# Kernel optimization log

Measured on AMD Instinct MI355X. Metric: run time of the kernel, lower is better.

The kernel has to match this reference:

```python
import math
import jax, jax.numpy as jnp
import numpy as np

B, S, D, H = 2, 2048, 1024, 16
HD = D // H  # 64


def setup_inputs() -> dict:
    key = jax.random.key(0)
    k = jax.random.split(key, 8)
    x = jax.random.normal(k[0], (B, S, D), dtype=jnp.float32)
    # RoPE tables: inv_freq over half dim, emb = concat(freqs, freqs)
    inv_freq = 1.0 / (10000.0 ** (jnp.arange(0, HD, 2, dtype=jnp.float32) / HD))
    pos = jnp.arange(S, dtype=jnp.float32)
    freqs = pos[:, None] * inv_freq[None, :]            # [S, HD/2]
    emb = jnp.concatenate([freqs, freqs], axis=-1)      # [S, HD]
    cos = jnp.cos(emb)[:, None, :]                      # [S, 1, HD] broadcasts over [B,S,H,HD]
    sin = jnp.sin(emb)[:, None, :]
    # causal additive mask [1, 1, S, S]
    neg = jnp.finfo(jnp.float32).min
    mask = jnp.where(jnp.tril(jnp.ones((S, S), dtype=bool)), 0.0, neg)[None, None]
    scale = 0.02
    wq = jax.random.normal(k[1], (D, D), dtype=jnp.float32) * scale
    wk = jax.random.normal(k[2], (D, D), dtype=jnp.float32) * scale
    wv = jax.random.normal(k[3], (D, D), dtype=jnp.float32) * scale
    wo = jax.random.normal(k[4], (D, D), dtype=jnp.float32) * scale
    return {"x": x, "cos": cos, "sin": sin, "mask": mask,
            "wq": wq, "wk": wk, "wv": wv, "wo": wo}


def rotate_half(t):
    t1, t2 = t[..., : t.shape[-1] // 2], t[..., t.shape[-1] // 2:]
    return jnp.concatenate([-t2, t1], axis=-1)


def reference(x, cos, sin, mask, wq, wk, wv, wo):
    b, s, d = x.shape
    # torch nn.Linear: y = x @ W^T  (W is [out, in])
    q = (x @ wq.T).reshape(b, s, H, HD)
    kk = (x @ wk.T).reshape(b, s, H, HD)
    v = (x @ wv.T).reshape(b, s, H, HD)
    q = q * cos + rotate_half(q) * sin
    kk = kk * cos + rotate_half(kk) * sin
    q = q.transpose(0, 2, 1, 3)   # [b, h, s, hd]
    kk = kk.transpose(0, 2, 1, 3)
    v = v.transpose(0, 2, 1, 3)
    scores = jnp.einsum('bhqd,bhkd->bhqk', q, kk) / math.sqrt(HD)
    scores = scores + mask
    probs = jax.nn.softmax(scores.astype(jnp.float32), axis=-1).astype(q.dtype)
    out = jnp.einsum('bhqk,bhkd->bhqd', probs, v)
    out = out.transpose(0, 2, 1, 3).reshape(b, s, d)
    return out @ wo.T
```

## Files before the change

### kernel.cpp

```cpp
#include <hip/hip_runtime.h>
#include <hip/hip_bf16.h>

typedef __hip_bfloat16 bf16;
typedef unsigned short u16;
typedef __attribute__((ext_vector_type(8))) short short8;
typedef __attribute__((ext_vector_type(4))) float floatx4;

constexpr int B_ = 2, S_ = 2048, D_ = 1024, H_ = 16, HD_ = 64;
constexpr int QT = 64, KT = 64, PAD = 72;
constexpr int NQT = S_ / QT;
constexpr int GK = 1024, BK = 64;

__device__ inline float b2f(u16 u) {
    union { unsigned int i; float f; } v; v.i = ((unsigned int)u) << 16; return v.f;
}
__device__ inline u16 f2b(float f) {
    bf16 h = __float2bfloat16(f); return *(u16*)&h;
}

__device__ inline void gl16(const u16* g, u16* l) {
    __builtin_amdgcn_global_load_lds(
        (const __attribute__((address_space(1))) unsigned int*)g,
        (__attribute__((address_space(3))) unsigned int*)l, 16, 0, 0);
}

__global__ __launch_bounds__(256) void cvt_kernel(
    const float* __restrict__ x,  const float* __restrict__ wq,
    const float* __restrict__ wk, const float* __restrict__ wv,
    const float* __restrict__ wo,
    u16* __restrict__ Xb, u16* __restrict__ Wb)
{
    const size_t c = (size_t)blockIdx.x * 256 + threadIdx.x;
    const float* src; u16* dst; size_t off;
    if (c < (size_t)(1 << 19)) { src = x; dst = Xb; off = c; }
    else {
        const size_t w = c - (1 << 19);
        const int wi = (int)(w >> 17);
        off = w & ((1 << 17) - 1);
        src = (wi == 0) ? wq : (wi == 1) ? wk : (wi == 2) ? wv : wo;
        dst = Wb + ((size_t)wi << 20);
    }
    const float4 a = *(const float4*)(src + off * 8);
    const float4 b = *(const float4*)(src + off * 8 + 4);
    ushort4 u0; u0.x = f2b(a.x); u0.y = f2b(a.y); u0.z = f2b(a.z); u0.w = f2b(a.w);
    ushort4 u1; u1.x = f2b(b.x); u1.y = f2b(b.y); u1.z = f2b(b.z); u1.w = f2b(b.w);
    *(ushort4*)(dst + off * 8)     = u0;
    *(ushort4*)(dst + off * 8 + 4) = u1;
}

template <typename TC, int SCATTER, int ROPE, int BN>
__global__ __launch_bounds__(256) void gemm_async(
    const u16* __restrict__ A, const u16* __restrict__ Wb,
    const float* __restrict__ cosp, const float* __restrict__ sinp,
    TC* __restrict__ C0, TC* __restrict__ C1, TC* __restrict__ C2, int N)
{
    constexpr int NT = BN / 32;

    int x, y, z;
    {
        const int xcd = blockIdx.x & 7, idx = blockIdx.x >> 3;
        y = (xcd & 3) * 8 + (idx & 7);
        if (BN == 128) {
            const int xz = (xcd >> 2) * 12 + (idx >> 3);
            x = xz & 7; z = xz >> 3;
        } else {
            x = (xcd >> 2) * 8 + (idx >> 3);
            z = 0;
        }
    }

    const u16* W = Wb + ((size_t)z << 20);
    TC*        C = (z == 0) ? C0 : (z == 1 ? C1 : C2);

    __shared__ __align__(16) u16 As[128 * BK];
    __shared__ __align__(16) u16 Bs[BN * BK];

    const int tid  = threadIdx.x;
    const int wave = tid >> 6, lane = tid & 63;
    const int quad = lane >> 4, l16 = lane & 15;
    const int wm = wave >> 1, wn = wave & 1;
    const int m0 = y * 128, n0 = x * BN;

    const int srl = lane >> 3;
    const int sc  = (lane & 7) ^ srl;

    floatx4 acc[4][NT] = {};

    for (int k0 = 0; k0 < GK; k0 += BK) {
        __syncthreads();
#pragma unroll
        for (int j = 0; j < 4; ++j) {
            const int rb = wave * 32 + j * 8;
            gl16(A + (size_t)(m0 + rb + srl) * GK + k0 + sc * 8, &As[rb * BK]);
        }
#pragma unroll
        for (int j = 0; j < BN / 32; ++j) {
            const int rb = wave * (BN / 4) + j * 8;
            gl16(W + (size_t)(n0 + rb + srl) * GK + k0 + sc * 8, &Bs[rb * BK]);
        }
        __syncthreads();

#pragma unroll
        for (int ks = 0; ks < 2; ++ks) {
            short8 af[4], bfr[NT];
#pragma unroll
            for (int mt = 0; mt < 4; ++mt) {
                const int R = wm * 64 + mt * 16 + l16;
                af[mt] = *(const short8*)&As[R * BK + (((ks * 4 + quad) ^ (l16 & 7)) * 8)];
            }
#pragma unroll
            for (int nt = 0; nt < NT; ++nt) {
                const int R = wn * (BN / 2) + nt * 16 + l16;
                bfr[nt] = *(const short8*)&Bs[R * BK + (((ks * 4 + quad) ^ (l16 & 7)) * 8)];
            }
#pragma unroll
            for (int mt = 0; mt < 4; ++mt)
#pragma unroll
                for (int nt = 0; nt < NT; ++nt)
                    acc[mt][nt] = __builtin_amdgcn_mfma_f32_16x16x32_bf16(
                        af[mt], bfr[nt], acc[mt][nt], 0, 0, 0);
        }
    }

    if (ROPE && z < 2) {
        float* Cs = (float*)As;
        float* Sn = (float*)Bs;
        const int s0 = m0 & (S_ - 1);
        const int bq = m0 >> 11;
        __syncthreads();
        {
            const int rr = tid >> 1;
            const int cc = (tid & 1) * 16;
            const float4* cp = (const float4*)(cosp + (size_t)(s0 + rr) * HD_ + cc);
            const float4* sp = (const float4*)(sinp + (size_t)(s0 + rr) * HD_ + cc);
            float4* cd = (float4*)&Cs[rr * 32 + cc];
            float4* sd = (float4*)&Sn[rr * 32 + cc];
            cd[0] = cp[0]; cd[1] = cp[1]; cd[2] = cp[2]; cd[3] = cp[3];
            sd[0] = sp[0]; sd[1] = sp[1]; sd[2] = sp[2]; sd[3] = sp[3];
        }
        __syncthreads();

        const float scale = (z == 0) ? 0.125f * 1.44269504f : 1.0f;
        const int h = (n0 >> 6) + wn;
#pragma unroll
        for (int mt = 0; mt < 4; ++mt)
#pragma unroll
            for (int r = 0; r < 4; ++r) {
                const int mr = wm * 64 + mt * 16 + quad * 4 + r;
                const size_t base = ((size_t)(bq * H_ + h) * S_ + s0 + mr) << 6;
#pragma unroll
                for (int np = 0; np < 2; ++np) {
                    const int d = np * 16 + l16;
                    const float c1 = Cs[mr * 32 + d];
                    const float s1 = Sn[mr * 32 + d];
                    const float q0 = acc[mt][np][r], q1 = acc[mt][np + 2][r];
                    ((bf16*)C)[base + d]      = __float2bfloat16((q0 * c1 - q1 * s1) * scale);
                    ((bf16*)C)[base + d + 32] = __float2bfloat16((q1 * c1 + q0 * s1) * scale);
                }
            }
    } else if (SCATTER) {
        const int s0 = m0 & (S_ - 1);
        const int bq = m0 >> 11;
        const int h  = (n0 >> 6) + wn;
        const int bh = bq * H_ + h;
#pragma unroll
        for (int mt = 0; mt < 4; ++mt)
#pragma unroll
            for (int nt = 0; nt < NT; ++nt) {
                const int hd = nt * 16 + l16;
                const int sb = s0 + wm * 64 + mt * 16 + quad * 4;
                ushort4 pk;
                pk.x = f2b(acc[mt][nt][0]); pk.y = f2b(acc[mt][nt][1]);
                pk.z = f2b(acc[mt][nt][2]); pk.w = f2b(acc[mt][nt][3]);
                *(ushort4*)&((u16*)C)[((size_t)(bh * HD_ + hd) << 11) + sb] = pk;
            }
    } else {
#pragma unroll
        for (int mt = 0; mt < 4; ++mt)
#pragma unroll
            for (int nt = 0; nt < NT; ++nt)
#pragma unroll
                for (int r = 0; r < 4; ++r) {
                    const int m = m0 + wm * 64 + mt * 16 + quad * 4 + r;
                    const int n = n0 + wn * (BN / 2) + nt * 16 + l16;
                    ((float*)C)[(size_t)m * N + n] = acc[mt][nt][r];
                }
    }
}

__global__ __launch_bounds__(256) void fa_kernel(
    const u16* __restrict__ Qg, const u16* __restrict__ Kg, const u16* __restrict__ Vt,
    bf16* __restrict__ Og)
{
    __shared__ __align__(16) u16 Kt[2][KT * PAD];
    __shared__ __align__(16) u16 Vs[2][HD_ * PAD];
    __shared__ __align__(16) u16 Pt[4 * 16 * PAD];

    const int flat = blockIdx.x;
    const int bx = flat >> 5;
    const int bh = flat & 31;
    const int b  = bh >> 4, h = bh & 15;
    const int tid  = threadIdx.x;
    const int wave = tid >> 6, lane = tid & 63;
    const int quad = lane >> 4, l16 = lane & 15;
    const int srow = tid >> 2, scol = (tid & 3) * 16;

    for (int half = 0; half < 2; ++half) {
        const int qt = half ? (NQT - 1 - bx) : bx;
        const int qb = qt * QT;

        const u16* qrow = Qg + ((size_t)bh * S_ + qb + wave * 16 + l16) * HD_;
        const short8 aq0 = *(const short8*)(qrow + quad * 8);
        const short8 aq1 = *(const short8*)(qrow + 32 + quad * 8);

        floatx4 oacc[4] = {{0,0,0,0},{0,0,0,0},{0,0,0,0},{0,0,0,0}};
        float lsum = 0.f;

        __syncthreads();
        {
            const u16* kp = Kg + ((size_t)bh * S_ + srow) * HD_ + scol;
            *(short8*)&Kt[0][srow * PAD + scol]     = *(const short8*)kp;
            *(short8*)&Kt[0][srow * PAD + scol + 8] = *(const short8*)(kp + 8);
            const u16* vp = Vt + ((size_t)bh * HD_ + srow) * S_ + scol;
            *(short8*)&Vs[0][srow * PAD + scol]     = *(const short8*)vp;
            *(short8*)&Vs[0][srow * PAD + scol + 8] = *(const short8*)(vp + 8);
        }
        __syncthreads();

        for (int it = 0; it <= qt; ++it) {
            const int  cur = it & 1;
            const bool pf  = (it < qt);
            short8 nk0, nk1, nv0, nv1;
            if (pf) {
                const int kb = (it + 1) * KT;
                const u16* kp = Kg + ((size_t)bh * S_ + kb + srow) * HD_ + scol;
                nk0 = *(const short8*)kp; nk1 = *(const short8*)(kp + 8);
                const u16* vp = Vt + ((size_t)bh * HD_ + srow) * S_ + kb + scol;
                nv0 = *(const short8*)vp; nv1 = *(const short8*)(vp + 8);
            }

            floatx4 sacc[4] = {{0,0,0,0},{0,0,0,0},{0,0,0,0},{0,0,0,0}};
#pragma unroll
            for (int kt = 0; kt < 4; ++kt) {
                const short8 bk0 = *(const short8*)&Kt[cur][(kt * 16 + l16) * PAD + quad * 8];
                const short8 bk1 = *(const short8*)&Kt[cur][(kt * 16 + l16) * PAD + 32 + quad * 8];
                sacc[kt] = __builtin_amdgcn_mfma_f32_16x16x32_bf16(bk0, aq0, sacc[kt], 0, 0, 0);
                sacc[kt] = __builtin_amdgcn_mfma_f32_16x16x32_bf16(bk1, aq1, sacc[kt], 0, 0, 0);
            }

            if (it == qt) {
                const int ql = wave * 16 + l16;
#pragma unroll
                for (int kt = 0; kt < 4; ++kt)
#pragma unroll
                    for (int r = 0; r < 4; ++r)
                        if (kt * 16 + quad * 4 + r > ql) sacc[kt][r] = -1.0e38f;
            }

            float rs = 0.f;
#pragma unroll
            for (int kt = 0; kt < 4; ++kt) {
                const float e0 = __builtin_amdgcn_exp2f(sacc[kt][0]);
                const float e1 = __builtin_amdgcn_exp2f(sacc[kt][1]);
                const float e2 = __builtin_amdgcn_exp2f(sacc[kt][2]);
                const float e3 = __builtin_amdgcn_exp2f(sacc[kt][3]);
                rs += (e0 + e1) + (e2 + e3);
                ushort4 pk; pk.x = f2b(e0); pk.y = f2b(e1); pk.z = f2b(e2); pk.w = f2b(e3);
                *(ushort4*)&Pt[(wave * 16 + l16) * PAD + kt * 16 + quad * 4] = pk;
            }
            rs += __shfl_xor(rs, 16);
            rs += __shfl_xor(rs, 32);
            lsum += rs;

            const short8 ap0 = *(const short8*)&Pt[(wave * 16 + l16) * PAD + quad * 8];
            const short8 ap1 = *(const short8*)&Pt[(wave * 16 + l16) * PAD + 32 + quad * 8];

#pragma unroll
            for (int dt = 0; dt < 4; ++dt) {
                const short8 bv0 = *(const short8*)&Vs[cur][(dt * 16 + l16) * PAD + quad * 8];
                const short8 bv1 = *(const short8*)&Vs[cur][(dt * 16 + l16) * PAD + 32 + quad * 8];
                oacc[dt] = __builtin_amdgcn_mfma_f32_16x16x32_bf16(bv0, ap0, oacc[dt], 0, 0, 0);
                oacc[dt] = __builtin_amdgcn_mfma_f32_16x16x32_bf16(bv1, ap1, oacc[dt], 0, 0, 0);
            }

            if (pf) {
                const int nb = cur ^ 1;
                *(short8*)&Kt[nb][srow * PAD + scol]     = nk0;
                *(short8*)&Kt[nb][srow * PAD + scol + 8] = nk1;
                *(short8*)&Vs[nb][srow * PAD + scol]     = nv0;
                *(short8*)&Vs[nb][srow * PAD + scol + 8] = nv1;
            }
            __syncthreads();
        }

        const float inv = 1.0f / lsum;
        bf16* orow = Og + ((size_t)(b * S_ + qb + wave * 16 + l16)) * D_ + h * HD_;
#pragma unroll
        for (int dt = 0; dt < 4; ++dt) {
            ushort4 pk;
            pk.x = f2b(oacc[dt][0] * inv);
            pk.y = f2b(oacc[dt][1] * inv);
            pk.z = f2b(oacc[dt][2] * inv);
            pk.w = f2b(oacc[dt][3] * inv);
            *(ushort4*)((u16*)orow + dt * 16 + quad * 4) = pk;
        }
    }
}

extern "C" void kernel_launch(void* const* d_in, const int* in_sizes, int n_in,
                              void* d_out, int out_size, void* d_ws, size_t ws_size,
                              hipStream_t stream)
{
    const float* x    = (const float*)d_in[0];
    const float* cosp = (const float*)d_in[1];
    const float* sinp = (const float*)d_in[2];
    const float* wq   = (const float*)d_in[4];
    const float* wk   = (const float*)d_in[5];
    const float* wv   = (const float*)d_in[6];
    const float* wo   = (const float*)d_in[7];
    float* out = (float*)d_out;

    u16* w0 = (u16*)d_ws;
    const size_t NE = (size_t)B_ * S_ * D_;
    u16* Qb  = w0;
    u16* Kb  = w0 + NE;
    u16* Vtb = w0 + 2 * NE;
    u16* Xb  = w0 + 3 * NE;
    u16* Wb  = w0 + 4 * NE;
    u16* Ab  = Xb;
    u16* Wob = Wb + 3 * (1 << 20);

    cvt_kernel<<<4096, 256, 0, stream>>>(x, wq, wk, wv, wo, Xb, Wb);

    gemm_async<bf16, 1, 1, 128><<<768, 256, 0, stream>>>(
        Xb, Wb, cosp, sinp, (bf16*)Qb, (bf16*)Kb, (bf16*)Vtb, D_);

    fa_kernel<<<dim3((NQT / 2) * 32, 1, 1), 256, 0, stream>>>(Qb, Kb, Vtb, (bf16*)Ab);

    gemm_async<float, 0, 0, 64><<<512, 256, 0, stream>>>(
        Ab, Wob, cosp, sinp, out, out, out, D_);
}
```

Measured before the change: 197.6 us.

## Double-buffer GEMM K-loop and fuse Q/K/V head tiles in one block

The GEMM is rewritten to use a 32-wide K step with two LDS buffers, so the load of the next K tile is issued before the MFMAs on the current one and each iteration needs one barrier instead of two. The QKV projection now gives each block one head's 64 columns from all three weight matrices (Q, K and V together), so every A tile is loaded once for all three. RoPE for Q and K and the transposed V store all happen in one shared epilogue. The launch goes from 768 to 512 blocks. In exchange, the K loop has twice as many iterations, and the larger per-thread accumulator set in the fused kernel may cut occupancy.

```diff
diff --git a/kernel.cpp b/kernel.cpp
--- a/kernel.cpp
+++ b/kernel.cpp
@@ -9,7 +9,7 @@
 constexpr int B_ = 2, S_ = 2048, D_ = 1024, H_ = 16, HD_ = 64;
 constexpr int QT = 64, KT = 64, PAD = 72;
 constexpr int NQT = S_ / QT;
-constexpr int GK = 1024, BK = 64;
+constexpr int GK = 1024;
 
 __device__ inline float b2f(u16 u) {
     union { unsigned int i; float f; } v; v.i = ((unsigned int)u) << 16; return v.f;
@@ -48,85 +48,87 @@
     *(ushort4*)(dst + off * 8 + 4) = u1;
 }
 
-template <typename TC, int SCATTER, int ROPE, int BN>
-__global__ __launch_bounds__(256) void gemm_async(
+template <int NW, int ROPE, typename TC>
+__global__ __launch_bounds__(256) void gemm_fused(
     const u16* __restrict__ A, const u16* __restrict__ Wb,
     const float* __restrict__ cosp, const float* __restrict__ sinp,
-    TC* __restrict__ C0, TC* __restrict__ C1, TC* __restrict__ C2, int N)
+    TC* __restrict__ C0, TC* __restrict__ C1, TC* __restrict__ C2)
 {
-    constexpr int NT = BN / 32;
-
-    int x, y, z;
-    {
-        const int xcd = blockIdx.x & 7, idx = blockIdx.x >> 3;
-        y = (xcd & 3) * 8 + (idx & 7);
-        if (BN == 128) {
-            const int xz = (xcd >> 2) * 12 + (idx >> 3);
-            x = xz & 7; z = xz >> 3;
-        } else {
-            x = (xcd >> 2) * 8 + (idx >> 3);
-            z = 0;
-        }
-    }
-
-    const u16* W = Wb + ((size_t)z << 20);
-    TC*        C = (z == 0) ? C0 : (z == 1 ? C1 : C2);
-
-    __shared__ __align__(16) u16 As[128 * BK];
-    __shared__ __align__(16) u16 Bs[BN * BK];
-
-    const int tid  = threadIdx.x;
+    constexpr int AS_E = 128 * 32;
+    constexpr int BS_E = NW * 64 * 32;
+    __shared__ __align__(16) u16 As[2][AS_E];
+    __shared__ __align__(16) u16 Bs[2][BS_E];
+
+    const int bid = blockIdx.x;
+    const int xcd = bid & 7, idx = bid >> 3;
+    const int y = xcd * 4 + (idx & 3);
+    const int x = idx >> 2;
+
+    const int tid = threadIdx.x;
     const int wave = tid >> 6, lane = tid & 63;
     const int quad = lane >> 4, l16 = lane & 15;
     const int wm = wave >> 1, wn = wave & 1;
-    const int m0 = y * 128, n0 = x * BN;
-
-    const int srl = lane >> 3;
-    const int sc  = (lane & 7) ^ srl;
-
-    floatx4 acc[4][NT] = {};
-
-    for (int k0 = 0; k0 < GK; k0 += BK) {
-        __syncthreads();
-#pragma unroll
-        for (int j = 0; j < 4; ++j) {
-            const int rb = wave * 32 + j * 8;
-            gl16(A + (size_t)(m0 + rb + srl) * GK + k0 + sc * 8, &As[rb * BK]);
-        }
-#pragma unroll
-        for (int j = 0; j < BN / 32; ++j) {
-            const int rb = wave * (BN / 4) + j * 8;
-            gl16(W + (size_t)(n0 + rb + srl) * GK + k0 + sc * 8, &Bs[rb * BK]);
-        }
-        __syncthreads();
-
-#pragma unroll
-        for (int ks = 0; ks < 2; ++ks) {
-            short8 af[4], bfr[NT];
-#pragma unroll
-            for (int mt = 0; mt < 4; ++mt) {
-                const int R = wm * 64 + mt * 16 + l16;
-                af[mt] = *(const short8*)&As[R * BK + (((ks * 4 + quad) ^ (l16 & 7)) * 8)];
-            }
-#pragma unroll
-            for (int nt = 0; nt < NT; ++nt) {
-                const int R = wn * (BN / 2) + nt * 16 + l16;
-                bfr[nt] = *(const short8*)&Bs[R * BK + (((ks * 4 + quad) ^ (l16 & 7)) * 8)];
-            }
-#pragma unroll
-            for (int mt = 0; mt < 4; ++mt)
-#pragma unroll
-                for (int nt = 0; nt < NT; ++nt)
-                    acc[mt][nt] = __builtin_amdgcn_mfma_f32_16x16x32_bf16(
-                        af[mt], bfr[nt], acc[mt][nt], 0, 0, 0);
-        }
+    const int m0 = y * 128, n0 = x * 64;
+
+    const int srw = lane >> 2;
+    const int scn = (lane & 3) ^ (srw & 3);
+
+    floatx4 acc[4][NW][2] = {};
+
+    auto stage = [&](int k0, int bufi) {
+#pragma unroll
+        for (int j = 0; j < 2; ++j) {
+            const int rb = wave * 32 + j * 16;
+            gl16(A + (size_t)(m0 + rb + srw) * GK + k0 + scn * 8, &As[bufi][rb * 32]);
+        }
+        if (NW == 3) {
+#pragma unroll
+            for (int j = 0; j < 3; ++j) {
+                const int rb = wave * 48 + j * 16;
+                const int w  = rb >> 6, rin = rb & 63;
+                gl16(Wb + ((size_t)w << 20) + (size_t)(n0 + rin + srw) * GK + k0 + scn * 8,
+                     &Bs[bufi][rb * 32]);
+            }
+        } else {
+            const int rb = wave * 16;
+            gl16(Wb + (size_t)(n0 + rb + srw) * GK + k0 + scn * 8, &Bs[bufi][rb * 32]);
+        }
+    };
+
+    stage(0, 0);
+    for (int it = 0; it < 32; ++it) {
+        __syncthreads();
+        if (it + 1 < 32) stage((it + 1) * 32, (it + 1) & 1);
+        const int cur = it & 1;
+
+        short8 af[4];
+#pragma unroll
+        for (int mt = 0; mt < 4; ++mt) {
+            const int R = wm * 64 + mt * 16 + l16;
+            af[mt] = *(const short8*)&As[cur][R * 32 + ((quad ^ (R & 3)) * 8)];
+        }
+        short8 bfr[NW][2];
+#pragma unroll
+        for (int w = 0; w < NW; ++w)
+#pragma unroll
+            for (int nt = 0; nt < 2; ++nt) {
+                const int Rb = w * 64 + nt * 32 + wn * 16 + l16;
+                bfr[w][nt] = *(const short8*)&Bs[cur][Rb * 32 + ((quad ^ (Rb & 3)) * 8)];
+            }
+#pragma unroll
+        for (int mt = 0; mt < 4; ++mt)
+#pragma unroll
+            for (int w = 0; w < NW; ++w)
+#pragma unroll
+                for (int nt = 0; nt < 2; ++nt)
+                    acc[mt][w][nt] = __builtin_amdgcn_mfma_f32_16x16x32_bf16(
+                        af[mt], bfr[w][nt], acc[mt][w][nt], 0, 0, 0);
     }
 
-    if (ROPE && z < 2) {
-        float* Cs = (float*)As;
-        float* Sn = (float*)Bs;
-        const int s0 = m0 & (S_ - 1);
-        const int bq = m0 >> 11;
+    if (ROPE) {
+        float* Cs = (float*)&As[0][0];
+        float* Sn = (float*)&Bs[0][0];
+        const int s0 = m0 & (S_ - 1), bq = m0 >> 11, h = x;
         __syncthreads();
         {
             const int rr = tid >> 1;
@@ -140,51 +142,46 @@
         }
         __syncthreads();
 
-        const float scale = (z == 0) ? 0.125f * 1.44269504f : 1.0f;
-        const int h = (n0 >> 6) + wn;
+        const float QSC = 0.125f * 1.44269504f;
+        const int dlo = wn * 16 + l16;
+        const int bh  = bq * H_ + h;
+#pragma unroll
+        for (int mt = 0; mt < 4; ++mt) {
+#pragma unroll
+            for (int r = 0; r < 4; ++r) {
+                const int sr = wm * 64 + mt * 16 + quad * 4 + r;
+                const float c1 = Cs[sr * 32 + dlo];
+                const float s1 = Sn[sr * 32 + dlo];
+                const size_t base = ((size_t)bh * S_ + s0 + sr) << 6;
+                const float q0 = acc[mt][0][0][r], q1 = acc[mt][0][1][r];
+                ((bf16*)C0)[base + dlo]      = __float2bfloat16((q0 * c1 - q1 * s1) * QSC);
+                ((bf16*)C0)[base + dlo + 32] = __float2bfloat16((q1 * c1 + q0 * s1) * QSC);
+                const float k0v = acc[mt][1][0][r], k1v = acc[mt][1][1][r];
+                ((bf16*)C1)[base + dlo]      = __float2bfloat16(k0v * c1 - k1v * s1);
+                ((bf16*)C1)[base + dlo + 32] = __float2bfloat16(k1v * c1 + k0v * s1);
+            }
+#pragma unroll
+            for (int nt = 0; nt < 2; ++nt) {
+                const int d  = nt * 32 + dlo;
+                const int sb = (m0 & (S_ - 1)) + wm * 64 + mt * 16 + quad * 4;
+                ushort4 pk;
+                pk.x = f2b(acc[mt][2][nt][0]); pk.y = f2b(acc[mt][2][nt][1]);
+                pk.z = f2b(acc[mt][2][nt][2]); pk.w = f2b(acc[mt][2][nt][3]);
+                *(ushort4*)&((u16*)C2)[((size_t)(bh * HD_ + d) << 11) + sb] = pk;
+            }
+        }
+    } else {
 #pragma unroll
         for (int mt = 0; mt < 4; ++mt)
 #pragma unroll
-            for (int r = 0; r < 4; ++r) {
-                const int mr = wm * 64 + mt * 16 + quad * 4 + r;
-                const size_t base = ((size_t)(bq * H_ + h) * S_ + s0 + mr) << 6;
-#pragma unroll
-                for (int np = 0; np < 2; ++np) {
-                    const int d = np * 16 + l16;
-                    const float c1 = Cs[mr * 32 + d];
-                    const float s1 = Sn[mr * 32 + d];
-                    const float q0 = acc[mt][np][r], q1 = acc[mt][np + 2][r];
-                    ((bf16*)C)[base + d]      = __float2bfloat16((q0 * c1 - q1 * s1) * scale);
-                    ((bf16*)C)[base + d + 32] = __float2bfloat16((q1 * c1 + q0 * s1) * scale);
-                }
-            }
-    } else if (SCATTER) {
-        const int s0 = m0 & (S_ - 1);
-        const int bq = m0 >> 11;
-        const int h  = (n0 >> 6) + wn;
-        const int bh = bq * H_ + h;
-#pragma unroll
-        for (int mt = 0; mt < 4; ++mt)
-#pragma unroll
-            for (int nt = 0; nt < NT; ++nt) {
-                const int hd = nt * 16 + l16;
-                const int sb = s0 + wm * 64 + mt * 16 + quad * 4;
-                ushort4 pk;
-                pk.x = f2b(acc[mt][nt][0]); pk.y = f2b(acc[mt][nt][1]);
-                pk.z = f2b(acc[mt][nt][2]); pk.w = f2b(acc[mt][nt][3]);
-                *(ushort4*)&((u16*)C)[((size_t)(bh * HD_ + hd) << 11) + sb] = pk;
-            }
-    } else {
-#pragma unroll
-        for (int mt = 0; mt < 4; ++mt)
-#pragma unroll
-            for (int nt = 0; nt < NT; ++nt)
+            for (int nt = 0; nt < 2; ++nt) {
+                const int n = n0 + nt * 32 + wn * 16 + l16;
 #pragma unroll
                 for (int r = 0; r < 4; ++r) {
                     const int m = m0 + wm * 64 + mt * 16 + quad * 4 + r;
-                    const int n = n0 + wn * (BN / 2) + nt * 16 + l16;
-                    ((float*)C)[(size_t)m * N + n] = acc[mt][nt][r];
+                    ((float*)C0)[(size_t)m * D_ + n] = acc[mt][0][nt][r];
                 }
+            }
     }
 }
 
@@ -332,11 +329,11 @@
 
     cvt_kernel<<<4096, 256, 0, stream>>>(x, wq, wk, wv, wo, Xb, Wb);
 
-    gemm_async<bf16, 1, 1, 128><<<768, 256, 0, stream>>>(
-        Xb, Wb, cosp, sinp, (bf16*)Qb, (bf16*)Kb, (bf16*)Vtb, D_);
+    gemm_fused<3, 1, bf16><<<512, 256, 0, stream>>>(
+        Xb, Wb, cosp, sinp, (bf16*)Qb, (bf16*)Kb, (bf16*)Vtb);
 
     fa_kernel<<<dim3((NQT / 2) * 32, 1, 1), 256, 0, stream>>>(Qb, Kb, Vtb, (bf16*)Ab);
 
-    gemm_async<float, 0, 0, 64><<<512, 256, 0, stream>>>(
-        Ab, Wob, cosp, sinp, out, out, out, D_);
-}
+    gemm_fused<1, 0, float><<<512, 256, 0, stream>>>(
+        Ab, Wob, cosp, sinp, out, out, out);
+}
```

Result: slower. 203.5 us (+3.0%).
